# Kernel optimization log

Measured on AMD Instinct MI355X. Metric: run time of the kernel, lower is better.

## Reference

```python
import jax, jax.numpy as jnp
import numpy as np

H = 8      # head_nums
D = 64     # head_planes
SCALE = D ** -0.5


def setup_inputs() -> dict:
    key = jax.random.key(0)
    ks = jax.random.split(key, 7)
    B, Nq, Nkv = 2, 2048, 2048
    Cq, Ck, I = 1024, 768, H * D
    return {
        "x": jax.random.normal(ks[0], (B, Nq, Cq), jnp.float32),
        "context": jax.random.normal(ks[1], (B, Nkv, Ck), jnp.float32),
        "Wq": jax.random.normal(ks[2], (Cq, I), jnp.float32) * (Cq ** -0.5),
        "Wk": jax.random.normal(ks[3], (Ck, I), jnp.float32) * (Ck ** -0.5),
        "Wv": jax.random.normal(ks[4], (Ck, I), jnp.float32) * (Ck ** -0.5),
        "Wo": jax.random.normal(ks[5], (I, Cq), jnp.float32) * (I ** -0.5),
        "bo": jnp.zeros((Cq,), jnp.float32),
    }


def reference(x, context, Wq, Wk, Wv, Wo, bo):
    B, Nq, _ = x.shape
    Nkv = context.shape[1]
    # projections (bias-free, as in to_q/to_k/to_v)
    q = (x @ Wq).reshape(B, Nq, H, D)        # b i h d
    k = (context @ Wk).reshape(B, Nkv, H, D)  # b j h d
    v = (context @ Wv).reshape(B, Nkv, H, D)
    # scaled dot-product attention, full [B,H,Nq,Nkv] scores as in original
    sim = jnp.einsum('bihd,bjhd->bhij', q, k) * SCALE
    attn = jax.nn.softmax(sim, axis=-1)
    out = jnp.einsum('bhij,bjhd->bihd', attn, v).reshape(B, Nq, H * D)
    # to_out linear (dropout_prob=0.0 -> identity)
    return out @ Wo + bo
```

## Files before the change

kernel.cpp:

```cpp
#include <hip/hip_runtime.h>
#include <hip/hip_bf16.h>

typedef __hip_bfloat16 bf16;
typedef __attribute__((ext_vector_type(8))) short short8;
typedef __attribute__((ext_vector_type(4))) float f32x4;

#define MFMA16(a, b, c) __builtin_amdgcn_mfma_f32_16x16x32_bf16((a), (b), (c), 0, 0, 0)

#define BATCH 2
#define NQ 2048
#define NKV 2048
#define HEADS 8
#define DHEAD 64
#define CQ 1024
#define CK 768
#define IDIM 512
#define SCALE 0.125f

__device__ __forceinline__ short8 ld8(const bf16* p) {
    return *(const short8*)p;
}

__device__ __forceinline__ void async_ld16(const bf16* g, bf16* l) {
    __builtin_amdgcn_global_load_lds((__attribute__((address_space(1))) const void*)g,
                                     (__attribute__((address_space(3))) void*)l,
                                     16, 0, 0);
}

__global__ __launch_bounds__(256) void prologue(
    const float* __restrict__ x, const float* __restrict__ ctx,
    const float* __restrict__ Wq, const float* __restrict__ Wk,
    const float* __restrict__ Wv, const float* __restrict__ Wo,
    bf16* __restrict__ Xb, bf16* __restrict__ Cb,
    bf16* __restrict__ WqT, bf16* __restrict__ WkT,
    bf16* __restrict__ WvT, bf16* __restrict__ WoT) {
    __shared__ float tile[64][65];
    const int t = threadIdx.x;
    const int bx = blockIdx.x;

    if (bx < 3584) {
        int idx = bx * 256 + t;
        const int NX8 = (4096 * 1024) / 8;
        const float4* srcp;
        bf16* dstp;
        if (idx < NX8) {
            srcp = (const float4*)x + (size_t)idx * 2;
            dstp = Xb + (size_t)idx * 8;
        } else {
            int j = idx - NX8;
            srcp = (const float4*)ctx + (size_t)j * 2;
            dstp = Cb + (size_t)j * 8;
        }
        float4 v0 = srcp[0], v1 = srcp[1];
        bf16 tmp[8] = {__float2bfloat16(v0.x), __float2bfloat16(v0.y),
                       __float2bfloat16(v0.z), __float2bfloat16(v0.w),
                       __float2bfloat16(v1.x), __float2bfloat16(v1.y),
                       __float2bfloat16(v1.z), __float2bfloat16(v1.w)};
        *(short8*)dstp = *(short8*)tmp;
        return;
    }

    int tb = bx - 3584;
    const float* src; bf16* dst; int R, C, ti;
    if (tb < 128)      { src = Wq; dst = WqT; R = 1024; C = 512;  ti = tb; }
    else if (tb < 224) { src = Wk; dst = WkT; R = 768;  C = 512;  ti = tb - 128; }
    else if (tb < 320) { src = Wv; dst = WvT; R = 768;  C = 512;  ti = tb - 224; }
    else               { src = Wo; dst = WoT; R = 512;  C = 1024; ti = tb - 320; }
    const int tilesC = C >> 6;
    const int tr = ti / tilesC, tc = ti - tr * tilesC;

    {
        int row = t >> 4;
        int c4 = (t & 15) * 4;
#pragma unroll
        for (int p = 0; p < 4; ++p) {
            float4 v = *(const float4*)&src[(size_t)(tr * 64 + p * 16 + row) * C + tc * 64 + c4];
            tile[p * 16 + row][c4 + 0] = v.x;
            tile[p * 16 + row][c4 + 1] = v.y;
            tile[p * 16 + row][c4 + 2] = v.z;
            tile[p * 16 + row][c4 + 3] = v.w;
        }
    }
    __syncthreads();
    {
        int oc = t >> 2;
        int r0 = (t & 3) * 16;
        bf16 tmp[16];
#pragma unroll
        for (int j = 0; j < 16; ++j)
            tmp[j] = __float2bfloat16(tile[r0 + j][oc]);
        bf16* dp = dst + (size_t)(tc * 64 + oc) * R + tr * 64 + r0;
        *(short8*)dp = *(short8*)&tmp[0];
        *(short8*)(dp + 8) = *(short8*)&tmp[8];
    }
}

__global__ __launch_bounds__(256) void qkv_gemm(
    const bf16* __restrict__ Xb, const bf16* __restrict__ Cb,
    const bf16* __restrict__ WqT, const bf16* __restrict__ WkT,
    const bf16* __restrict__ WvT,
    bf16* __restrict__ Qb, bf16* __restrict__ Kb, bf16* __restrict__ Vt) {
    __shared__ bf16 At[2][64 * 32];
    __shared__ bf16 Bts[2][128 * 32];

    const int z = blockIdx.z;
    const bf16* A  = (z == 0) ? Xb : Cb;
    const bf16* Bt = (z == 0) ? WqT : (z == 1) ? WkT : WvT;
    const int K = (z == 0) ? 1024 : 768;

    const int t = threadIdx.x;
    const int wave = t >> 6;
    const int lane = t & 63;
    const int n15 = lane & 15;
    const int quad = lane >> 4;
    const int wm = wave >> 1;
    const int wn = wave & 1;
    const int bm = blockIdx.y;
    const int bn = blockIdx.x;

    f32x4 acc[2][4] = {};

    const bf16* Ablk = A + (size_t)bm * 64 * K;
    const bf16* Bblk = Bt + (size_t)bn * 128 * K;

    const int arow = t >> 2, ak8 = t & 3;
    const int brow0 = t >> 2, bk80 = t & 3;
    const int brow1 = (256 + t) >> 2, bk81 = t & 3;

    async_ld16(Ablk + arow * K + ak8 * 8, &At[0][t * 8]);
    async_ld16(Bblk + brow0 * K + bk80 * 8, &Bts[0][t * 8]);
    async_ld16(Bblk + brow1 * K + bk81 * 8, &Bts[0][(256 + t) * 8]);
    __syncthreads();

    for (int k0 = 0; k0 < K; k0 += 32) {
        const int p = (k0 >> 5) & 1;
        if (k0 + 32 < K) {
            const int q = p ^ 1;
            const int kn = k0 + 32;
            async_ld16(Ablk + arow * K + kn + ak8 * 8, &At[q][t * 8]);
            async_ld16(Bblk + brow0 * K + kn + bk80 * 8, &Bts[q][t * 8]);
            async_ld16(Bblk + brow1 * K + kn + bk81 * 8, &Bts[q][(256 + t) * 8]);
        }

        short8 af[2], bfr[4];
#pragma unroll
        for (int mt = 0; mt < 2; ++mt)
            af[mt] = ld8(&At[p][(wm * 32 + mt * 16 + n15) * 32 + quad * 8]);
#pragma unroll
        for (int nt = 0; nt < 4; ++nt)
            bfr[nt] = ld8(&Bts[p][(wn * 64 + nt * 16 + n15) * 32 + quad * 8]);

#pragma unroll
        for (int mt = 0; mt < 2; ++mt)
#pragma unroll
            for (int nt = 0; nt < 4; ++nt)
                acc[mt][nt] = MFMA16(af[mt], bfr[nt], acc[mt][nt]);

        __syncthreads();
    }

    bf16* C = (z == 0) ? Qb : (z == 1) ? Kb : Vt;
#pragma unroll
    for (int mt = 0; mt < 2; ++mt) {
#pragma unroll
        for (int nt = 0; nt < 4; ++nt) {
            int col = bn * 128 + wn * 64 + nt * 16 + n15;
#pragma unroll
            for (int r = 0; r < 4; ++r) {
                int row = bm * 64 + wm * 32 + mt * 16 + quad * 4 + r;
                bf16 v = __float2bfloat16(acc[mt][nt][r]);
                if (z < 2) {
                    C[(size_t)row * 512 + col] = v;
                } else {
                    int b = row >> 11, j = row & 2047;
                    int h = col >> 6, d = col & 63;
                    C[(size_t)(((b << 3) + h) * 64 + d) * 2048 + j] = v;
                }
            }
        }
    }
}

__global__ __launch_bounds__(256) void out_gemm(const bf16* __restrict__ A,
                                                const bf16* __restrict__ Bt,
                                                const float* __restrict__ bias,
                                                float* __restrict__ C) {
    const int K = 512, N = 1024;
    __shared__ bf16 At[2][64 * 32];
    __shared__ bf16 Bts[2][128 * 32];

    const int t = threadIdx.x;
    const int wave = t >> 6;
    const int lane = t & 63;
    const int n15 = lane & 15;
    const int quad = lane >> 4;
    const int wm = wave >> 1;
    const int wn = wave & 1;
    const int bm = blockIdx.y;
    const int bn = blockIdx.x;

    f32x4 acc[2][4] = {};

    const bf16* Ablk = A + (size_t)bm * 64 * K;
    const bf16* Bblk = Bt + (size_t)bn * 128 * K;

    const int arow = t >> 2, ak8 = t & 3;
    const int brow1 = (256 + t) >> 2;

    async_ld16(Ablk + arow * K + ak8 * 8, &At[0][t * 8]);
    async_ld16(Bblk + arow * K + ak8 * 8, &Bts[0][t * 8]);
    async_ld16(Bblk + brow1 * K + ak8 * 8, &Bts[0][(256 + t) * 8]);
    __syncthreads();

    for (int k0 = 0; k0 < K; k0 += 32) {
        const int p = (k0 >> 5) & 1;
        if (k0 + 32 < K) {
            const int q = p ^ 1;
            const int kn = k0 + 32;
            async_ld16(Ablk + arow * K + kn + ak8 * 8, &At[q][t * 8]);
            async_ld16(Bblk + arow * K + kn + ak8 * 8, &Bts[q][t * 8]);
            async_ld16(Bblk + brow1 * K + kn + ak8 * 8, &Bts[q][(256 + t) * 8]);
        }

        short8 af[2], bfr[4];
#pragma unroll
        for (int mt = 0; mt < 2; ++mt)
            af[mt] = ld8(&At[p][(wm * 32 + mt * 16 + n15) * 32 + quad * 8]);
#pragma unroll
        for (int nt = 0; nt < 4; ++nt)
            bfr[nt] = ld8(&Bts[p][(wn * 64 + nt * 16 + n15) * 32 + quad * 8]);

#pragma unroll
        for (int mt = 0; mt < 2; ++mt)
#pragma unroll
            for (int nt = 0; nt < 4; ++nt)
                acc[mt][nt] = MFMA16(af[mt], bfr[nt], acc[mt][nt]);

        __syncthreads();
    }

#pragma unroll
    for (int mt = 0; mt < 2; ++mt) {
#pragma unroll
        for (int nt = 0; nt < 4; ++nt) {
            int col = bn * 128 + wn * 64 + nt * 16 + n15;
            float bv = bias[col];
#pragma unroll
            for (int r = 0; r < 4; ++r) {
                int row = bm * 64 + wm * 32 + mt * 16 + quad * 4 + r;
                C[(size_t)row * N + col] = acc[mt][nt][r] + bv;
            }
        }
    }
}

__global__ __launch_bounds__(256) void flash_attn(const bf16* __restrict__ Q,
                                                  const bf16* __restrict__ K,
                                                  const bf16* __restrict__ Vt,
                                                  bf16* __restrict__ O) {
    __shared__ bf16 Kt[2][64 * 64];
    __shared__ bf16 Vte[2][64 * 64];
    __shared__ bf16 Pa[4][16 * 72];

    const int t = threadIdx.x;
    const int wave = t >> 6;
    const int lane = t & 63;
    const int n15 = lane & 15;
    const int quad = lane >> 4;

    const int L = blockIdx.x;
    const int bh = L & 15;
    const int b = bh >> 3, h = bh & 7;
    const int q0 = (L >> 4) * 64;
    const int qw = q0 + wave * 16;

    const bf16* Qp = Q + ((size_t)(b * NQ + qw) * IDIM + h * DHEAD);
    const bf16* Kp = K + ((size_t)b * NKV * IDIM + h * DHEAD);
    const bf16* Vp = Vt + (size_t)((b * HEADS + h) * DHEAD) * NKV;
    bf16* Pw = Pa[wave];

    short8 qa0 = ld8(Qp + n15 * IDIM + quad * 8);
    short8 qa1 = ld8(Qp + n15 * IDIM + 32 + quad * 8);

    const int s0 = wave * 128 + lane;
    const int s1 = s0 + 64;
    const int r0 = s0 >> 3, c0 = (s0 & 7) ^ (r0 & 7);
    const int r1 = s1 >> 3, c1 = (s1 & 7) ^ (r1 & 7);
    const bf16* kg0 = Kp + r0 * IDIM + c0 * 8;
    const bf16* kg1 = Kp + r1 * IDIM + c1 * 8;
    const bf16* vg0 = Vp + (size_t)r0 * NKV + c0 * 8;
    const bf16* vg1 = Vp + (size_t)r1 * NKV + c1 * 8;

    f32x4 o[4] = {};
    float lsum = 0.f;
    const int sw = n15 & 7;

    async_ld16(kg0, &Kt[0][s0 * 8]);
    async_ld16(kg1, &Kt[0][s1 * 8]);
    async_ld16(vg0, &Vte[0][s0 * 8]);
    async_ld16(vg1, &Vte[0][s1 * 8]);
    __syncthreads();

    for (int key0 = 0; key0 < NKV; key0 += 64) {
        const int p = (key0 >> 6) & 1;
        if (key0 + 64 < NKV) {
            const int q = p ^ 1;
            const int kn = key0 + 64;
            async_ld16(kg0 + (size_t)kn * IDIM, &Kt[q][s0 * 8]);
            async_ld16(kg1 + (size_t)kn * IDIM, &Kt[q][s1 * 8]);
            async_ld16(vg0 + kn, &Vte[q][s0 * 8]);
            async_ld16(vg1 + kn, &Vte[q][s1 * 8]);
        }

        f32x4 s[4] = {};
#pragma unroll
        for (int su = 0; su < 4; ++su) {
            const bf16* kr = &Kt[p][(su * 16 + n15) * 64];
            short8 ka0 = ld8(kr + ((quad ^ sw) * 8));
            short8 ka1 = ld8(kr + (((4 + quad) ^ sw) * 8));
            s[su] = MFMA16(ka0, qa0, s[su]);
            s[su] = MFMA16(ka1, qa1, s[su]);
        }

#pragma unroll
        for (int su = 0; su < 4; ++su) {
            float p0 = __expf(s[su][0] * SCALE);
            float p1 = __expf(s[su][1] * SCALE);
            float p2 = __expf(s[su][2] * SCALE);
            float p3 = __expf(s[su][3] * SCALE);
            lsum += (p0 + p1) + (p2 + p3);
            bf16 pk[4] = {__float2bfloat16(p0), __float2bfloat16(p1),
                          __float2bfloat16(p2), __float2bfloat16(p3)};
            *(uint2*)&Pw[n15 * 72 + su * 16 + quad * 4] = *(uint2*)pk;
        }
        asm volatile("s_waitcnt lgkmcnt(0)" ::: "memory");

        short8 pb0 = ld8(&Pw[n15 * 72 + quad * 8]);
        short8 pb1 = ld8(&Pw[n15 * 72 + 32 + quad * 8]);

#pragma unroll
        for (int d4 = 0; d4 < 4; ++d4) {
            const bf16* vr = &Vte[p][(d4 * 16 + n15) * 64];
            short8 va0 = ld8(vr + ((quad ^ sw) * 8));
            short8 va1 = ld8(vr + (((4 + quad) ^ sw) * 8));
            o[d4] = MFMA16(va0, pb0, o[d4]);
            o[d4] = MFMA16(va1, pb1, o[d4]);
        }
        __syncthreads();
    }

    lsum += __shfl_xor(lsum, 16, 64);
    lsum += __shfl_xor(lsum, 32, 64);
    float inv = 1.0f / lsum;

#pragma unroll
    for (int d4 = 0; d4 < 4; ++d4) {
        bf16 pk[4];
#pragma unroll
        for (int r = 0; r < 4; ++r) pk[r] = __float2bfloat16(o[d4][r] * inv);
        *(uint2*)&Pw[n15 * 72 + d4 * 16 + quad * 4] = *(uint2*)pk;
    }
    __syncthreads();

    {
        int ql = t >> 2, seg = t & 3;
        const bf16* src = &Pa[ql >> 4][(ql & 15) * 72 + seg * 16];
        short8 a0 = ld8(src);
        short8 a1 = ld8(src + 8);
        bf16* dst = O + ((size_t)(b * NQ + q0 + ql) * IDIM + h * DHEAD + seg * 16);
        *(short8*)dst = a0;
        *(short8*)(dst + 8) = a1;
    }
}

extern "C" void kernel_launch(void* const* d_in, const int* in_sizes, int n_in,
                              void* d_out, int out_size, void* d_ws, size_t ws_size,
                              hipStream_t stream) {
    (void)in_sizes; (void)n_in; (void)out_size; (void)ws_size;

    const float* x   = (const float*)d_in[0];
    const float* ctx = (const float*)d_in[1];
    const float* Wq  = (const float*)d_in[2];
    const float* Wk  = (const float*)d_in[3];
    const float* Wv  = (const float*)d_in[4];
    const float* Wo  = (const float*)d_in[5];
    const float* bo  = (const float*)d_in[6];
    float* out = (float*)d_out;

    char* ws = (char*)d_ws;
    bf16* Xb  = (bf16*)(ws + 0);
    bf16* Cb  = (bf16*)(ws + 8388608);
    bf16* WqT = (bf16*)(ws + 14680064);
    bf16* WkT = (bf16*)(ws + 15728640);
    bf16* WvT = (bf16*)(ws + 16515072);
    bf16* WoT = (bf16*)(ws + 17301504);
    bf16* Qb  = (bf16*)(ws + 18350080);
    bf16* Kb  = (bf16*)(ws + 22544384);
    bf16* Vt  = (bf16*)(ws + 26738688);
    bf16* Ob  = (bf16*)(ws + 30932992);

    prologue<<<4032, 256, 0, stream>>>(x, ctx, Wq, Wk, Wv, Wo,
                                       Xb, Cb, WqT, WkT, WvT, WoT);

    qkv_gemm<<<dim3(4, 64, 3), 256, 0, stream>>>(Xb, Cb, WqT, WkT, WvT, Qb, Kb, Vt);

    flash_attn<<<512, 256, 0, stream>>>(Qb, Kb, Vt, Ob);

    out_gemm<<<dim3(8, 64), 256, 0, stream>>>(Ob, WoT, bo, out);
}
```

Measured before the change: 165.5 us.

## Widen GEMM K-tile with XOR-swizzled LDS and double flash-attn query rows per wave

The QKV and output GEMMs now stage 64-wide K tiles, half as many barrier iterations as before, using an XOR swizzle on the LDS row chunks to avoid bank conflicts. Flash attention now has each wave handle 32 query rows instead of 16, so every K/V fragment loaded from LDS feeds twice as many MFMAs. The grid drops to 256 blocks with launch bounds of one block per SIMD. The trade-off is more registers and LDS per block and only 256 blocks to spread across the GPU's compute units, which can leave some idle.

```diff
diff --git a/kernel.cpp b/kernel.cpp
--- a/kernel.cpp
+++ b/kernel.cpp
@@ -100,8 +100,8 @@
     const bf16* __restrict__ WqT, const bf16* __restrict__ WkT,
     const bf16* __restrict__ WvT,
     bf16* __restrict__ Qb, bf16* __restrict__ Kb, bf16* __restrict__ Vt) {
-    __shared__ bf16 At[2][64 * 32];
-    __shared__ bf16 Bts[2][128 * 32];
+    __shared__ bf16 At[2][64 * 64];
+    __shared__ bf16 Bts[2][128 * 64];
 
     const int z = blockIdx.z;
     const bf16* A  = (z == 0) ? Xb : Cb;
@@ -123,38 +123,58 @@
     const bf16* Ablk = A + (size_t)bm * 64 * K;
     const bf16* Bblk = Bt + (size_t)bn * 128 * K;
 
-    const int arow = t >> 2, ak8 = t & 3;
-    const int brow0 = t >> 2, bk80 = t & 3;
-    const int brow1 = (256 + t) >> 2, bk81 = t & 3;
-
-    async_ld16(Ablk + arow * K + ak8 * 8, &At[0][t * 8]);
-    async_ld16(Bblk + brow0 * K + bk80 * 8, &Bts[0][t * 8]);
-    async_ld16(Bblk + brow1 * K + bk81 * 8, &Bts[0][(256 + t) * 8]);
+    int ar[2], ac[2], br[4], bc[4];
+#pragma unroll
+    for (int i = 0; i < 2; ++i) {
+        int g = i * 256 + t;
+        ar[i] = g >> 3; ac[i] = ((g & 7) ^ (ar[i] & 7)) * 8;
+    }
+#pragma unroll
+    for (int i = 0; i < 4; ++i) {
+        int g = i * 256 + t;
+        br[i] = g >> 3; bc[i] = ((g & 7) ^ (br[i] & 7)) * 8;
+    }
+
+#pragma unroll
+    for (int i = 0; i < 2; ++i)
+        async_ld16(Ablk + ar[i] * K + ac[i], &At[0][(i * 256 + t) * 8]);
+#pragma unroll
+    for (int i = 0; i < 4; ++i)
+        async_ld16(Bblk + br[i] * K + bc[i], &Bts[0][(i * 256 + t) * 8]);
     __syncthreads();
 
-    for (int k0 = 0; k0 < K; k0 += 32) {
-        const int p = (k0 >> 5) & 1;
-        if (k0 + 32 < K) {
+    for (int k0 = 0; k0 < K; k0 += 64) {
+        const int p = (k0 >> 6) & 1;
+        if (k0 + 64 < K) {
             const int q = p ^ 1;
-            const int kn = k0 + 32;
-            async_ld16(Ablk + arow * K + kn + ak8 * 8, &At[q][t * 8]);
-            async_ld16(Bblk + brow0 * K + kn + bk80 * 8, &Bts[q][t * 8]);
-            async_ld16(Bblk + brow1 * K + kn + bk81 * 8, &Bts[q][(256 + t) * 8]);
-        }
-
-        short8 af[2], bfr[4];
-#pragma unroll
-        for (int mt = 0; mt < 2; ++mt)
-            af[mt] = ld8(&At[p][(wm * 32 + mt * 16 + n15) * 32 + quad * 8]);
-#pragma unroll
-        for (int nt = 0; nt < 4; ++nt)
-            bfr[nt] = ld8(&Bts[p][(wn * 64 + nt * 16 + n15) * 32 + quad * 8]);
-
-#pragma unroll
-        for (int mt = 0; mt < 2; ++mt)
-#pragma unroll
-            for (int nt = 0; nt < 4; ++nt)
-                acc[mt][nt] = MFMA16(af[mt], bfr[nt], acc[mt][nt]);
+            const int kn = k0 + 64;
+#pragma unroll
+            for (int i = 0; i < 2; ++i)
+                async_ld16(Ablk + ar[i] * K + kn + ac[i], &At[q][(i * 256 + t) * 8]);
+#pragma unroll
+            for (int i = 0; i < 4; ++i)
+                async_ld16(Bblk + br[i] * K + kn + bc[i], &Bts[q][(i * 256 + t) * 8]);
+        }
+
+#pragma unroll
+        for (int kh = 0; kh < 2; ++kh) {
+            short8 af[2], bfr[4];
+#pragma unroll
+            for (int mt = 0; mt < 2; ++mt) {
+                int R = wm * 32 + mt * 16 + n15;
+                af[mt] = ld8(&At[p][R * 64 + (((kh * 4 + quad) ^ (R & 7)) * 8)]);
+            }
+#pragma unroll
+            for (int nt = 0; nt < 4; ++nt) {
+                int R = wn * 64 + nt * 16 + n15;
+                bfr[nt] = ld8(&Bts[p][R * 64 + (((kh * 4 + quad) ^ (R & 7)) * 8)]);
+            }
+#pragma unroll
+            for (int mt = 0; mt < 2; ++mt)
+#pragma unroll
+                for (int nt = 0; nt < 4; ++nt)
+                    acc[mt][nt] = MFMA16(af[mt], bfr[nt], acc[mt][nt]);
+        }
 
         __syncthreads();
     }
@@ -186,8 +206,8 @@
                                                 const float* __restrict__ bias,
                                                 float* __restrict__ C) {
     const int K = 512, N = 1024;
-    __shared__ bf16 At[2][64 * 32];
-    __shared__ bf16 Bts[2][128 * 32];
+    __shared__ bf16 At[2][64 * 64];
+    __shared__ bf16 Bts[2][128 * 64];
 
     const int t = threadIdx.x;
     const int wave = t >> 6;
@@ -204,37 +224,58 @@
     const bf16* Ablk = A + (size_t)bm * 64 * K;
     const bf16* Bblk = Bt + (size_t)bn * 128 * K;
 
-    const int arow = t >> 2, ak8 = t & 3;
-    const int brow1 = (256 + t) >> 2;
-
-    async_ld16(Ablk + arow * K + ak8 * 8, &At[0][t * 8]);
-    async_ld16(Bblk + arow * K + ak8 * 8, &Bts[0][t * 8]);
-    async_ld16(Bblk + brow1 * K + ak8 * 8, &Bts[0][(256 + t) * 8]);
+    int ar[2], ac[2], br[4], bc[4];
+#pragma unroll
+    for (int i = 0; i < 2; ++i) {
+        int g = i * 256 + t;
+        ar[i] = g >> 3; ac[i] = ((g & 7) ^ (ar[i] & 7)) * 8;
+    }
+#pragma unroll
+    for (int i = 0; i < 4; ++i) {
+        int g = i * 256 + t;
+        br[i] = g >> 3; bc[i] = ((g & 7) ^ (br[i] & 7)) * 8;
+    }
+
+#pragma unroll
+    for (int i = 0; i < 2; ++i)
+        async_ld16(Ablk + ar[i] * K + ac[i], &At[0][(i * 256 + t) * 8]);
+#pragma unroll
+    for (int i = 0; i < 4; ++i)
+        async_ld16(Bblk + br[i] * K + bc[i], &Bts[0][(i * 256 + t) * 8]);
     __syncthreads();
 
-    for (int k0 = 0; k0 < K; k0 += 32) {
-        const int p = (k0 >> 5) & 1;
-        if (k0 + 32 < K) {
+    for (int k0 = 0; k0 < K; k0 += 64) {
+        const int p = (k0 >> 6) & 1;
+        if (k0 + 64 < K) {
             const int q = p ^ 1;
-            const int kn = k0 + 32;
-            async_ld16(Ablk + arow * K + kn + ak8 * 8, &At[q][t * 8]);
-            async_ld16(Bblk + arow * K + kn + ak8 * 8, &Bts[q][t * 8]);
-            async_ld16(Bblk + brow1 * K + kn + ak8 * 8, &Bts[q][(256 + t) * 8]);
-        }
-
-        short8 af[2], bfr[4];
-#pragma unroll
-        for (int mt = 0; mt < 2; ++mt)
-            af[mt] = ld8(&At[p][(wm * 32 + mt * 16 + n15) * 32 + quad * 8]);
-#pragma unroll
-        for (int nt = 0; nt < 4; ++nt)
-            bfr[nt] = ld8(&Bts[p][(wn * 64 + nt * 16 + n15) * 32 + quad * 8]);
-
-#pragma unroll
-        for (int mt = 0; mt < 2; ++mt)
-#pragma unroll
-            for (int nt = 0; nt < 4; ++nt)
-                acc[mt][nt] = MFMA16(af[mt], bfr[nt], acc[mt][nt]);
+            const int kn = k0 + 64;
+#pragma unroll
+            for (int i = 0; i < 2; ++i)
+                async_ld16(Ablk + ar[i] * K + kn + ac[i], &At[q][(i * 256 + t) * 8]);
+#pragma unroll
+            for (int i = 0; i < 4; ++i)
+                async_ld16(Bblk + br[i] * K + kn + bc[i], &Bts[q][(i * 256 + t) * 8]);
+        }
+
+#pragma unroll
+        for (int kh = 0; kh < 2; ++kh) {
+            short8 af[2], bfr[4];
+#pragma unroll
+            for (int mt = 0; mt < 2; ++mt) {
+                int R = wm * 32 + mt * 16 + n15;
+                af[mt] = ld8(&At[p][R * 64 + (((kh * 4 + quad) ^ (R & 7)) * 8)]);
+            }
+#pragma unroll
+            for (int nt = 0; nt < 4; ++nt) {
+                int R = wn * 64 + nt * 16 + n15;
+                bfr[nt] = ld8(&Bts[p][R * 64 + (((kh * 4 + quad) ^ (R & 7)) * 8)]);
+            }
+#pragma unroll
+            for (int mt = 0; mt < 2; ++mt)
+#pragma unroll
+                for (int nt = 0; nt < 4; ++nt)
+                    acc[mt][nt] = MFMA16(af[mt], bfr[nt], acc[mt][nt]);
+        }
 
         __syncthreads();
     }
@@ -254,13 +295,13 @@
     }
 }
 
-__global__ __launch_bounds__(256) void flash_attn(const bf16* __restrict__ Q,
-                                                  const bf16* __restrict__ K,
-                                                  const bf16* __restrict__ Vt,
-                                                  bf16* __restrict__ O) {
+__global__ __launch_bounds__(256, 1) void flash_attn(const bf16* __restrict__ Q,
+                                                     const bf16* __restrict__ K,
+                                                     const bf16* __restrict__ Vt,
+                                                     bf16* __restrict__ O) {
     __shared__ bf16 Kt[2][64 * 64];
     __shared__ bf16 Vte[2][64 * 64];
-    __shared__ bf16 Pa[4][16 * 72];
+    __shared__ bf16 Pa[4][32 * 72];
 
     const int t = threadIdx.x;
     const int wave = t >> 6;
@@ -271,16 +312,20 @@
     const int L = blockIdx.x;
     const int bh = L & 15;
     const int b = bh >> 3, h = bh & 7;
-    const int q0 = (L >> 4) * 64;
-    const int qw = q0 + wave * 16;
+    const int q0 = (L >> 4) * 128;
+    const int qw = q0 + wave * 32;
 
     const bf16* Qp = Q + ((size_t)(b * NQ + qw) * IDIM + h * DHEAD);
     const bf16* Kp = K + ((size_t)b * NKV * IDIM + h * DHEAD);
     const bf16* Vp = Vt + (size_t)((b * HEADS + h) * DHEAD) * NKV;
     bf16* Pw = Pa[wave];
 
-    short8 qa0 = ld8(Qp + n15 * IDIM + quad * 8);
-    short8 qa1 = ld8(Qp + n15 * IDIM + 32 + quad * 8);
+    short8 qa[2][2];
+#pragma unroll
+    for (int j = 0; j < 2; ++j)
+#pragma unroll
+        for (int kh = 0; kh < 2; ++kh)
+            qa[j][kh] = ld8(Qp + (j * 16 + n15) * IDIM + kh * 32 + quad * 8);
 
     const int s0 = wave * 128 + lane;
     const int s1 = s0 + 64;
@@ -291,8 +336,8 @@
     const bf16* vg0 = Vp + (size_t)r0 * NKV + c0 * 8;
     const bf16* vg1 = Vp + (size_t)r1 * NKV + c1 * 8;
 
-    f32x4 o[4] = {};
-    float lsum = 0.f;
+    f32x4 o[4][2] = {};
+    float lsum[2] = {0.f, 0.f};
     const int sw = n15 & 7;
 
     async_ld16(kg0, &Kt[0][s0 * 8]);
@@ -312,64 +357,85 @@
             async_ld16(vg1 + kn, &Vte[q][s1 * 8]);
         }
 
-        f32x4 s[4] = {};
+        f32x4 s[4][2] = {};
 #pragma unroll
         for (int su = 0; su < 4; ++su) {
             const bf16* kr = &Kt[p][(su * 16 + n15) * 64];
             short8 ka0 = ld8(kr + ((quad ^ sw) * 8));
             short8 ka1 = ld8(kr + (((4 + quad) ^ sw) * 8));
-            s[su] = MFMA16(ka0, qa0, s[su]);
-            s[su] = MFMA16(ka1, qa1, s[su]);
+#pragma unroll
+            for (int j = 0; j < 2; ++j) {
+                s[su][j] = MFMA16(ka0, qa[j][0], s[su][j]);
+                s[su][j] = MFMA16(ka1, qa[j][1], s[su][j]);
+            }
         }
 
 #pragma unroll
         for (int su = 0; su < 4; ++su) {
-            float p0 = __expf(s[su][0] * SCALE);
-            float p1 = __expf(s[su][1] * SCALE);
-            float p2 = __expf(s[su][2] * SCALE);
-            float p3 = __expf(s[su][3] * SCALE);
-            lsum += (p0 + p1) + (p2 + p3);
-            bf16 pk[4] = {__float2bfloat16(p0), __float2bfloat16(p1),
-                          __float2bfloat16(p2), __float2bfloat16(p3)};
-            *(uint2*)&Pw[n15 * 72 + su * 16 + quad * 4] = *(uint2*)pk;
+#pragma unroll
+            for (int j = 0; j < 2; ++j) {
+                float p0 = __expf(s[su][j][0] * SCALE);
+                float p1 = __expf(s[su][j][1] * SCALE);
+                float p2 = __expf(s[su][j][2] * SCALE);
+                float p3 = __expf(s[su][j][3] * SCALE);
+                lsum[j] += (p0 + p1) + (p2 + p3);
+                bf16 pk[4] = {__float2bfloat16(p0), __float2bfloat16(p1),
+                              __float2bfloat16(p2), __float2bfloat16(p3)};
+                *(uint2*)&Pw[(j * 16 + n15) * 72 + su * 16 + quad * 4] = *(uint2*)pk;
+            }
         }
         asm volatile("s_waitcnt lgkmcnt(0)" ::: "memory");
 
-        short8 pb0 = ld8(&Pw[n15 * 72 + quad * 8]);
-        short8 pb1 = ld8(&Pw[n15 * 72 + 32 + quad * 8]);
+        short8 pb[2][2];
+#pragma unroll
+        for (int j = 0; j < 2; ++j) {
+            pb[j][0] = ld8(&Pw[(j * 16 + n15) * 72 + quad * 8]);
+            pb[j][1] = ld8(&Pw[(j * 16 + n15) * 72 + 32 + quad * 8]);
+        }
 
 #pragma unroll
         for (int d4 = 0; d4 < 4; ++d4) {
             const bf16* vr = &Vte[p][(d4 * 16 + n15) * 64];
             short8 va0 = ld8(vr + ((quad ^ sw) * 8));
             short8 va1 = ld8(vr + (((4 + quad) ^ sw) * 8));
-            o[d4] = MFMA16(va0, pb0, o[d4]);
-            o[d4] = MFMA16(va1, pb1, o[d4]);
+#pragma unroll
+            for (int j = 0; j < 2; ++j) {
+                o[d4][j] = MFMA16(va0, pb[j][0], o[d4][j]);
+                o[d4][j] = MFMA16(va1, pb[j][1], o[d4][j]);
+            }
         }
         __syncthreads();
     }
 
-    lsum += __shfl_xor(lsum, 16, 64);
-    lsum += __shfl_xor(lsum, 32, 64);
-    float inv = 1.0f / lsum;
-
-#pragma unroll
-    for (int d4 = 0; d4 < 4; ++d4) {
-        bf16 pk[4];
-#pragma unroll
-        for (int r = 0; r < 4; ++r) pk[r] = __float2bfloat16(o[d4][r] * inv);
-        *(uint2*)&Pw[n15 * 72 + d4 * 16 + quad * 4] = *(uint2*)pk;
+#pragma unroll
+    for (int j = 0; j < 2; ++j) {
+        float lt = lsum[j];
+        lt += __shfl_xor(lt, 16, 64);
+        lt += __shfl_xor(lt, 32, 64);
+        float inv = 1.0f / lt;
+#pragma unroll
+        for (int d4 = 0; d4 < 4; ++d4) {
+            bf16 pk[4];
+#pragma unroll
+            for (int r = 0; r < 4; ++r)
+                pk[r] = __float2bfloat16(o[d4][j][r] * inv);
+            *(uint2*)&Pw[(j * 16 + n15) * 72 + d4 * 16 + quad * 4] = *(uint2*)pk;
+        }
     }
     __syncthreads();
 
     {
-        int ql = t >> 2, seg = t & 3;
-        const bf16* src = &Pa[ql >> 4][(ql & 15) * 72 + seg * 16];
+        int ql = t >> 1, seg = t & 1;
+        const bf16* src = &Pa[ql >> 5][(ql & 31) * 72 + seg * 32];
         short8 a0 = ld8(src);
         short8 a1 = ld8(src + 8);
-        bf16* dst = O + ((size_t)(b * NQ + q0 + ql) * IDIM + h * DHEAD + seg * 16);
+        short8 a2 = ld8(src + 16);
+        short8 a3 = ld8(src + 24);
+        bf16* dst = O + ((size_t)(b * NQ + q0 + ql) * IDIM + h * DHEAD + seg * 32);
         *(short8*)dst = a0;
         *(short8*)(dst + 8) = a1;
+        *(short8*)(dst + 16) = a2;
+        *(short8*)(dst + 24) = a3;
     }
 }
 
@@ -404,7 +470,7 @@
 
     qkv_gemm<<<dim3(4, 64, 3), 256, 0, stream>>>(Xb, Cb, WqT, WkT, WvT, Qb, Kb, Vt);
 
-    flash_attn<<<512, 256, 0, stream>>>(Qb, Kb, Vt, Ob);
+    flash_attn<<<256, 256, 0, stream>>>(Qb, Kb, Vt, Ob);
 
     out_gemm<<<dim3(8, 64), 256, 0, stream>>>(Ob, WoT, bo, out);
 }
```

Measured after the change: 167.0 us. About the same (+0.9%).
